# Performance work log

Hardware: AMD Instinct MI355X
Metric: run time of the kernel (lower is better)

## Reference

```python
import jax, jax.numpy as jnp
import numpy as np

BINARY_K = 64  # self.binary_k


def setup_inputs() -> dict:
    key = jax.random.key(0)
    ks = jax.random.split(key, 8)
    R, N, D, H = 8, 128, 512, 256
    obj_feats = jax.random.normal(ks[0], (R, N, D), dtype=jnp.float32)
    geo_feats = jax.random.normal(ks[1], (R, N, N, D), dtype=jnp.float32) * 0.1
    mask = jnp.ones((N, N), dtype=jnp.float32)
    mask = mask.at[jnp.arange(N), jnp.arange(N)].set(0.0)  # zero diagonal, as in forward()
    s1 = 1.0 / np.sqrt(D)
    s2 = 1.0 / np.sqrt(H)
    return {
        "obj_feats": obj_feats,
        "geo_feats": geo_feats,
        "mask": mask,
        "w1a": jax.random.normal(ks[2], (D, H), dtype=jnp.float32) * s1,
        "b1a": jnp.zeros((H,), dtype=jnp.float32),
        "w2a": jax.random.normal(ks[3], (H, 1), dtype=jnp.float32) * s2,
        "b2a": jnp.zeros((1,), dtype=jnp.float32),
        "w1b": jax.random.normal(ks[4], (D, H), dtype=jnp.float32) * s1,
        "b1b": jnp.zeros((H,), dtype=jnp.float32),
        "w2b": jax.random.normal(ks[5], (H, 1), dtype=jnp.float32) * s2,
        "b2b": jnp.zeros((1,), dtype=jnp.float32),
    }


def reference(obj_feats, geo_feats, mask, w1a, b1a, w2a, b2a, w1b, b1b, w2b, b2b):
    # pair_aware_perbatch (dropout = identity in eval mode)
    R, N, D = obj_feats.shape
    k = min(BINARY_K, N * N)

    # pairwise outer-product features + geometric features: [R, N, N, D]
    obj2obj = obj_feats[:, None, :, :] * obj_feats[:, :, None, :] + geo_feats

    # re_clf1 MLP scorer: D -> D/2 -> 1
    h = jax.nn.relu(jnp.einsum('rijd,dh->rijh', obj2obj, w1a) + b1a)
    logits = jnp.einsum('rijh,h->rij', h, w2a[:, 0]) + b2a[0]     # [R, N, N]
    o2o_logits = logits.reshape(R, N * N).sum(axis=0) / R          # [N*N]

    pair_probs = jax.nn.sigmoid(o2o_logits) * mask.ravel()
    _, topk_inds = jax.lax.top_k(pair_probs, k)                    # [k]

    # averaged pair features, gather topk
    a_obj2obj = obj2obj.reshape(R, N * N, D).sum(axis=0) / R       # [N*N, D]
    pair_feats = a_obj2obj[topk_inds]                              # [k, D]

    # pair-of-pair outer product + second MLP scorer
    p2p = pair_feats[None, :, :] * pair_feats[:, None, :]          # [k, k, D]
    h2 = jax.nn.relu(jnp.einsum('ijd,dh->ijh', p2p, w1b) + b1b)
    p2p_logits = jnp.einsum('ijh,h->ij', h2, w2b[:, 0]) + b2b[0]   # [k, k]

    return o2o_logits.reshape(N, N), p2p_logits, topk_inds
```

## Files before the change

### kernel.cpp

```cpp
#include <hip/hip_runtime.h>
#include <math.h>

typedef unsigned int u32;
typedef unsigned long long u64;
typedef unsigned short u16;
typedef short bf16x8 __attribute__((ext_vector_type(8)));
typedef float f32x4 __attribute__((ext_vector_type(4)));

#define RR 8
#define NN 128
#define DD 512
#define HH 256
#define KTOP 64
#define NCAND 256
#define NSEL 128

#define WS_LOGITS_OFF 0
#define WS_CAND_OFF   65536
#define WS_EXACT_OFF  66560
#define WS_CNT_OFF    67584
#define WS_TOPK_OFF   67600
#define WS_PF_OFF     67856
#define WS_WH_OFF     198928
#define WS_WL_OFF     461072

__device__ __forceinline__ u16 bf16rne(float x) {
    union { float f; u32 u; } v; v.f = x;
    u32 r = (v.u + 0x7fffu + ((v.u >> 16) & 1u)) >> 16;
    return (u16)r;
}
__device__ __forceinline__ float bf16tof(u16 h) {
    union { float f; u32 u; } v; v.u = ((u32)h) << 16; return v.f;
}
__device__ __forceinline__ u32 f32sort(float x) {
    union { float f; u32 u; } v; v.f = x;
    return v.u ^ ((v.u & 0x80000000u) ? 0xFFFFFFFFu : 0x80000000u);
}

__global__ __launch_bounds__(256) void k0_splitW(const float* __restrict__ W1,
                                                 u16* __restrict__ wh, u16* __restrict__ wl,
                                                 float* __restrict__ logits)
{
    if (blockIdx.x == 16) {
        float4 z = {0.f, 0.f, 0.f, 0.f};
        for (int t = threadIdx.x; t < 4096; t += 256)
            ((float4*)logits)[t] = z;
        return;
    }
    const int kc = blockIdx.x;
    const int h  = threadIdx.x;
    const int swz = (h >> 1) & 3;
    u16 rh[32], rl[32];
#pragma unroll
    for (int kk = 0; kk < 32; ++kk) {
        float a = W1[(size_t)(kc * 32 + kk) * HH + h];
        u16 hi = bf16rne(a);
        float lo = a - bf16tof(hi);
        rh[kk] = hi; rl[kk] = bf16rne(lo);
    }
    const size_t base = (size_t)kc * 8192 + (size_t)h * 32;
#pragma unroll
    for (int q = 0; q < 4; ++q) {
        uint4 ph, pl;
        ph.x = (u32)rh[q*8+0] | ((u32)rh[q*8+1] << 16);
        ph.y = (u32)rh[q*8+2] | ((u32)rh[q*8+3] << 16);
        ph.z = (u32)rh[q*8+4] | ((u32)rh[q*8+5] << 16);
        ph.w = (u32)rh[q*8+6] | ((u32)rh[q*8+7] << 16);
        pl.x = (u32)rl[q*8+0] | ((u32)rl[q*8+1] << 16);
        pl.y = (u32)rl[q*8+2] | ((u32)rl[q*8+3] << 16);
        pl.z = (u32)rl[q*8+4] | ((u32)rl[q*8+5] << 16);
        pl.w = (u32)rl[q*8+6] | ((u32)rl[q*8+7] << 16);
        const int qs = (q ^ swz) * 8;
        *(uint4*)&wh[base + qs] = ph;
        *(uint4*)&wl[base + qs] = pl;
    }
}

__global__ __launch_bounds__(256, 2) void k1_pair_mfma(
    const float* __restrict__ obj, const float* __restrict__ geo,
    const u16* __restrict__ wh, const u16* __restrict__ wl,
    const float* __restrict__ b1, const float* __restrict__ w2,
    float* __restrict__ logits_acc)
{
    const int jb = blockIdx.x, i = blockIdx.y, r = blockIdx.z;
    const int j0 = jb * 64;
    const int tid = threadIdx.x;
    const int lane = tid & 63, wv = tid >> 6;
    const int l15 = lane & 15, quad = lane >> 4;
    const int fsl = (quad ^ ((l15 >> 1) & 3)) * 8;

    __shared__ float sObjI[DD];
    __shared__ __align__(16) u16 sAh[64 * 32], sAl[64 * 32];
    __shared__ __align__(16) u16 sBh[256 * 32], sBl[256 * 32];

    const float* objI = obj + (size_t)(r * NN + i) * DD;
    for (int t = tid; t < DD; t += 256) sObjI[t] = objI[t];

    f32x4 acc[4][4];
#pragma unroll
    for (int mt = 0; mt < 4; ++mt)
#pragma unroll
        for (int nt = 0; nt < 4; ++nt) acc[mt][nt] = (f32x4){0.f, 0.f, 0.f, 0.f};

    const float* geoB = geo + ((size_t)(r * NN + i) * NN + j0) * DD;
    const float* objJ = obj + (size_t)(r * NN + j0) * DD;

    const int aj = tid >> 2;
    const int ak = (tid & 3) * 8;
    const int asl = ((tid & 3) ^ ((aj >> 1) & 3)) * 8;

    for (int kc = 0; kc < 16; ++kc) {
        const int k0 = kc * 32;
        __syncthreads();
        {
            const char* gh = (const char*)(wh + (size_t)kc * 8192);
            const char* gl = (const char*)(wl + (size_t)kc * 8192);
#pragma unroll
            for (int p = 0; p < 4; ++p) {
                const int off = (wv * 4 + p) * 1024;
                __builtin_amdgcn_global_load_lds(
                    (const __attribute__((address_space(1))) u32*)(gh + off + lane * 16),
                    (__attribute__((address_space(3))) u32*)((char*)sBh + off), 16, 0, 0);
                __builtin_amdgcn_global_load_lds(
                    (const __attribute__((address_space(1))) u32*)(gl + off + lane * 16),
                    (__attribute__((address_space(3))) u32*)((char*)sBl + off), 16, 0, 0);
            }
        }
        {
            float4 g0 = *(const float4*)(geoB + (size_t)aj * DD + k0 + ak);
            float4 g1 = *(const float4*)(geoB + (size_t)aj * DD + k0 + ak + 4);
            float4 o0 = *(const float4*)(objJ + (size_t)aj * DD + k0 + ak);
            float4 o1 = *(const float4*)(objJ + (size_t)aj * DD + k0 + ak + 4);
            float a[8];
            a[0] = fmaf(sObjI[k0+ak+0], o0.x, g0.x);
            a[1] = fmaf(sObjI[k0+ak+1], o0.y, g0.y);
            a[2] = fmaf(sObjI[k0+ak+2], o0.z, g0.z);
            a[3] = fmaf(sObjI[k0+ak+3], o0.w, g0.w);
            a[4] = fmaf(sObjI[k0+ak+4], o1.x, g1.x);
            a[5] = fmaf(sObjI[k0+ak+5], o1.y, g1.y);
            a[6] = fmaf(sObjI[k0+ak+6], o1.z, g1.z);
            a[7] = fmaf(sObjI[k0+ak+7], o1.w, g1.w);
            u16 hs[8], ls[8];
#pragma unroll
            for (int q = 0; q < 8; ++q) {
                hs[q] = bf16rne(a[q]);
                ls[q] = bf16rne(a[q] - bf16tof(hs[q]));
            }
            uint4 ph, pl;
            ph.x = (u32)hs[0] | ((u32)hs[1] << 16); ph.y = (u32)hs[2] | ((u32)hs[3] << 16);
            ph.z = (u32)hs[4] | ((u32)hs[5] << 16); ph.w = (u32)hs[6] | ((u32)hs[7] << 16);
            pl.x = (u32)ls[0] | ((u32)ls[1] << 16); pl.y = (u32)ls[2] | ((u32)ls[3] << 16);
            pl.z = (u32)ls[4] | ((u32)ls[5] << 16); pl.w = (u32)ls[6] | ((u32)ls[7] << 16);
            *(uint4*)&sAh[aj * 32 + asl] = ph;
            *(uint4*)&sAl[aj * 32 + asl] = pl;
        }
        __syncthreads();
        bf16x8 Bh[4], Bl[4], Ah[4], Al[4];
#pragma unroll
        for (int nt = 0; nt < 4; ++nt) {
            const int row = wv * 64 + nt * 16 + l15;
            Bh[nt] = *(const bf16x8*)&sBh[row * 32 + fsl];
            Bl[nt] = *(const bf16x8*)&sBl[row * 32 + fsl];
        }
#pragma unroll
        for (int mt = 0; mt < 4; ++mt) {
            const int row = mt * 16 + l15;
            Ah[mt] = *(const bf16x8*)&sAh[row * 32 + fsl];
            Al[mt] = *(const bf16x8*)&sAl[row * 32 + fsl];
        }
#pragma unroll
        for (int mt = 0; mt < 4; ++mt)
#pragma unroll
            for (int nt = 0; nt < 4; ++nt) {
                acc[mt][nt] = __builtin_amdgcn_mfma_f32_16x16x32_bf16(Ah[mt], Bh[nt], acc[mt][nt], 0, 0, 0);
                acc[mt][nt] = __builtin_amdgcn_mfma_f32_16x16x32_bf16(Ah[mt], Bl[nt], acc[mt][nt], 0, 0, 0);
                acc[mt][nt] = __builtin_amdgcn_mfma_f32_16x16x32_bf16(Al[mt], Bh[nt], acc[mt][nt], 0, 0, 0);
            }
    }
    float pr[4][4];
#pragma unroll
    for (int mt = 0; mt < 4; ++mt)
#pragma unroll
        for (int t = 0; t < 4; ++t) pr[mt][t] = 0.f;
#pragma unroll
    for (int nt = 0; nt < 4; ++nt) {
        const int h = wv * 64 + nt * 16 + l15;
        const float bb = b1[h], w = w2[h];
#pragma unroll
        for (int mt = 0; mt < 4; ++mt)
#pragma unroll
            for (int t = 0; t < 4; ++t)
                pr[mt][t] += fmaxf(acc[mt][nt][t] + bb, 0.f) * w;
    }
#pragma unroll
    for (int mt = 0; mt < 4; ++mt)
#pragma unroll
        for (int t = 0; t < 4; ++t) {
            float v = pr[mt][t];
            v += __shfl_xor(v, 1); v += __shfl_xor(v, 2);
            v += __shfl_xor(v, 4); v += __shfl_xor(v, 8);
            if (l15 == 0)
                atomicAdd(&logits_acc[i * NN + j0 + mt * 16 + quad * 4 + t], v);
        }
}

__global__ __launch_bounds__(1024) void k2_hist(
    const float* __restrict__ logits_acc, const float* __restrict__ mask,
    const float* __restrict__ b2a, float* __restrict__ out,
    int* __restrict__ cand, int* __restrict__ cnt_out)
{
    __shared__ u32 hist[16 * 256];
    __shared__ u32 sum1[256];
    __shared__ int sB1, sRem, sT16;
    __shared__ u32 sCnt;
    const int t = threadIdx.x;
    const int hb = (t >> 6) << 8;
    for (int b = t; b < 16 * 256; b += 1024) hist[b] = 0;
    if (t == 0) sCnt = 0;
    __syncthreads();
    const float bias = b2a[0];
    u32 skey[16];
#pragma unroll
    for (int e = 0; e < 16; ++e) {
        const int idx = e * 1024 + t;
        const float lg = logits_acc[idx] * 0.125f + bias;
        out[idx] = lg;
        u32 s = f32sort(lg);
        if (mask[idx] == 0.f) s = 0;
        skey[e] = s;
        atomicAdd(&hist[hb + (s >> 24)], 1u);
    }
    __syncthreads();
    if (t < 256) {
        u32 s = 0;
#pragma unroll
        for (int c = 0; c < 16; ++c) s += hist[c * 256 + t];
        sum1[t] = s;
    }
    __syncthreads();
    if (t == 0) {
        u32 cum = 0; int b = 255;
        for (; b > 0; --b) { u32 c = sum1[b]; if (cum + c >= (u32)NSEL) break; cum += c; }
        sB1 = b; sRem = NSEL - (int)cum;
    }
    __syncthreads();
    const int B1 = sB1;
    for (int b = t; b < 16 * 256; b += 1024) hist[b] = 0;
    __syncthreads();
#pragma unroll
    for (int e = 0; e < 16; ++e) {
        const u32 s = skey[e];
        if ((int)(s >> 24) == B1) atomicAdd(&hist[hb + ((s >> 16) & 0xFF)], 1u);
    }
    __syncthreads();
    if (t < 256) {
        u32 s = 0;
#pragma unroll
        for (int c = 0; c < 16; ++c) s += hist[c * 256 + t];
        sum1[t] = s;
    }
    __syncthreads();
    if (t == 0) {
        const int rem = sRem; u32 cum = 0; int b = 255;
        for (; b > 0; --b) { cum += sum1[b]; if ((int)cum >= rem) break; }
        sT16 = (B1 << 8) | b;
    }
    __syncthreads();
    const u32 T16 = (u32)sT16;
#pragma unroll
    for (int e = 0; e < 16; ++e) {
        const u32 s = skey[e];
        if (s != 0 && (s >> 16) >= T16) {
            const u32 pos = atomicAdd(&sCnt, 1u);
            if (pos < (u32)NCAND) cand[pos] = e * 1024 + t;
        }
    }
    __syncthreads();
    if (t == 0) *cnt_out = (int)(sCnt < (u32)NCAND ? sCnt : (u32)NCAND);
}

__global__ __launch_bounds__(256) void k5_exact(
    const float* __restrict__ obj, const float* __restrict__ geo,
    const float* __restrict__ W1, const float* __restrict__ b1,
    const float* __restrict__ w2, const float* __restrict__ b2a,
    const int* __restrict__ cand, const int* __restrict__ cnt_ptr,
    float* __restrict__ exact)
{
    const int c = blockIdx.x;
    if (c >= *cnt_ptr) { if (threadIdx.x == 0) exact[c] = -1e30f; return; }
    const int idx = cand[c];
    const int i = idx >> 7, j = idx & 127;
    const int t = threadIdx.x;
    __shared__ float sA[RR][DD];
    __shared__ float sRed[4];
    for (int f = t; f < RR * DD; f += 256) {
        const int r = f >> 9, k = f & 511;
        sA[r][k] = fmaf(obj[(size_t)(r * NN + i) * DD + k],
                        obj[(size_t)(r * NN + j) * DD + k],
                        geo[((size_t)(r * NN + i) * NN + j) * DD + k]);
    }
    __syncthreads();
    float hv[RR];
#pragma unroll
    for (int r = 0; r < RR; ++r) hv[r] = 0.f;
#pragma unroll 8
    for (int k = 0; k < DD; ++k) {
        const float w = W1[(size_t)k * HH + t];
#pragma unroll
        for (int r = 0; r < RR; ++r) hv[r] = fmaf(sA[r][k], w, hv[r]);
    }
    const float bb = b1[t], wv2 = w2[t];
    float p = 0.f;
#pragma unroll
    for (int r = 0; r < RR; ++r) p += fmaxf(hv[r] + bb, 0.f) * wv2;
#pragma unroll
    for (int off = 1; off < 64; off <<= 1) p += __shfl_xor(p, off);
    if ((t & 63) == 0) sRed[t >> 6] = p;
    __syncthreads();
    if (t == 0) exact[c] = (sRed[0] + sRed[1] + sRed[2] + sRed[3]) * 0.125f + b2a[0];
}

__global__ __launch_bounds__(256) void k_sortgather(
    const float* __restrict__ exact, const int* __restrict__ cand,
    const float* __restrict__ obj, const float* __restrict__ geo,
    float* __restrict__ out, float* __restrict__ pf)
{
    __shared__ u64 sKey[NCAND];
    const int t = threadIdx.x;
    {
        const float lg = exact[t];
        u32 ps = 0; u32 idx = 0x7FFFFFFFu;
        if (lg > -1e29f) {
            const float p = 1.f / (1.f + expf(-lg));
            ps = f32sort(p);
            idx = (u32)cand[t];
        }
        sKey[t] = ((u64)ps << 32) | (u64)(0xFFFFFFFFu - idx);
    }
    for (int k = 2; k <= NCAND; k <<= 1)
        for (int j = k >> 1; j > 0; j >>= 1) {
            __syncthreads();
            const int ixj = t ^ j;
            if (ixj > t) {
                const u64 a = sKey[t], b = sKey[ixj];
                if (((t & k) == 0) ? (a < b) : (a > b)) { sKey[t] = b; sKey[ixj] = a; }
            }
        }
    __syncthreads();
    const int tix = blockIdx.x;
    if (tix == 0 && t < KTOP) {
        const u32 oidx = 0xFFFFFFFFu - (u32)(sKey[t] & 0xFFFFFFFFull);
        out[20480 + t] = (float)oidx;
    }
    const int idx = (int)(0xFFFFFFFFu - (u32)(sKey[tix] & 0xFFFFFFFFull));
    const int i = idx >> 7, j = idx & 127;
    for (int dd = t; dd < DD; dd += 256) {
        float s = 0.f;
#pragma unroll
        for (int r = 0; r < RR; ++r) {
            const float oi = obj[(size_t)(r * NN + i) * DD + dd];
            const float oj = obj[(size_t)(r * NN + j) * DD + dd];
            const float g  = geo[((size_t)(r * NN + i) * NN + j) * DD + dd];
            s += oi * oj + g;
        }
        pf[tix * DD + dd] = s * 0.125f;
    }
}

__global__ __launch_bounds__(256) void k4_p2p(
    const float* __restrict__ pf, const float* __restrict__ W1,
    const float* __restrict__ b1, const float* __restrict__ w2,
    const float* __restrict__ b2, float* __restrict__ out)
{
    const int a = blockIdx.x;
    const int tid = threadIdx.x;
    const int lane = tid & 63, wv = tid >> 6;
    const int l15 = lane & 15, quad = lane >> 4;
    const int fsl = (quad ^ ((l15 >> 1) & 3)) * 8;

    __shared__ float sPfA[DD];
    __shared__ __align__(16) u16 sAh[64 * 32], sAl[64 * 32];
    __shared__ __align__(16) u16 sBh[256 * 32], sBl[256 * 32];
    __shared__ float sRed[4][64];

    const float* pfA = pf + (size_t)a * DD;
    for (int t = tid; t < DD; t += 256) sPfA[t] = pfA[t];

    f32x4 acc[4][4];
#pragma unroll
    for (int mt = 0; mt < 4; ++mt)
#pragma unroll
        for (int nt = 0; nt < 4; ++nt) acc[mt][nt] = (f32x4){0.f, 0.f, 0.f, 0.f};

    const int aj = tid >> 2;
    const int ak = (tid & 3) * 8;
    const int asl = ((tid & 3) ^ ((aj >> 1) & 3)) * 8;
    const int swzB = (tid >> 1) & 3;

    for (int kc = 0; kc < 16; ++kc) {
        const int k0 = kc * 32;
        __syncthreads();
        {
            u16 rh[32], rl[32];
#pragma unroll
            for (int kk = 0; kk < 32; ++kk) {
                float w = W1[(size_t)(k0 + kk) * HH + tid];
                u16 hi = bf16rne(w);
                rh[kk] = hi; rl[kk] = bf16rne(w - bf16tof(hi));
            }
#pragma unroll
            for (int q = 0; q < 4; ++q) {
                uint4 ph, pl;
                ph.x = (u32)rh[q*8+0] | ((u32)rh[q*8+1] << 16);
                ph.y = (u32)rh[q*8+2] | ((u32)rh[q*8+3] << 16);
                ph.z = (u32)rh[q*8+4] | ((u32)rh[q*8+5] << 16);
                ph.w = (u32)rh[q*8+6] | ((u32)rh[q*8+7] << 16);
                pl.x = (u32)rl[q*8+0] | ((u32)rl[q*8+1] << 16);
                pl.y = (u32)rl[q*8+2] | ((u32)rl[q*8+3] << 16);
                pl.z = (u32)rl[q*8+4] | ((u32)rl[q*8+5] << 16);
                pl.w = (u32)rl[q*8+6] | ((u32)rl[q*8+7] << 16);
                const int qs = (q ^ swzB) * 8;
                *(uint4*)&sBh[tid * 32 + qs] = ph;
                *(uint4*)&sBl[tid * 32 + qs] = pl;
            }
        }
        {
            float4 p0 = *(const float4*)(pf + (size_t)aj * DD + k0 + ak);
            float4 p1 = *(const float4*)(pf + (size_t)aj * DD + k0 + ak + 4);
            float av[8];
            av[0] = sPfA[k0+ak+0] * p0.x; av[1] = sPfA[k0+ak+1] * p0.y;
            av[2] = sPfA[k0+ak+2] * p0.z; av[3] = sPfA[k0+ak+3] * p0.w;
            av[4] = sPfA[k0+ak+4] * p1.x; av[5] = sPfA[k0+ak+5] * p1.y;
            av[6] = sPfA[k0+ak+6] * p1.z; av[7] = sPfA[k0+ak+7] * p1.w;
            u16 hs[8], ls[8];
#pragma unroll
            for (int q = 0; q < 8; ++q) {
                hs[q] = bf16rne(av[q]);
                ls[q] = bf16rne(av[q] - bf16tof(hs[q]));
            }
            uint4 ph, pl;
            ph.x = (u32)hs[0] | ((u32)hs[1] << 16); ph.y = (u32)hs[2] | ((u32)hs[3] << 16);
            ph.z = (u32)hs[4] | ((u32)hs[5] << 16); ph.w = (u32)hs[6] | ((u32)hs[7] << 16);
            pl.x = (u32)ls[0] | ((u32)ls[1] << 16); pl.y = (u32)ls[2] | ((u32)ls[3] << 16);
            pl.z = (u32)ls[4] | ((u32)ls[5] << 16); pl.w = (u32)ls[6] | ((u32)ls[7] << 16);
            *(uint4*)&sAh[aj * 32 + asl] = ph;
            *(uint4*)&sAl[aj * 32 + asl] = pl;
        }
        __syncthreads();
        bf16x8 Bh[4], Bl[4], Ah[4], Al[4];
#pragma unroll
        for (int nt = 0; nt < 4; ++nt) {
            const int row = wv * 64 + nt * 16 + l15;
            Bh[nt] = *(const bf16x8*)&sBh[row * 32 + fsl];
            Bl[nt] = *(const bf16x8*)&sBl[row * 32 + fsl];
        }
#pragma unroll
        for (int mt = 0; mt < 4; ++mt) {
            const int row = mt * 16 + l15;
            Ah[mt] = *(const bf16x8*)&sAh[row * 32 + fsl];
            Al[mt] = *(const bf16x8*)&sAl[row * 32 + fsl];
        }
#pragma unroll
        for (int mt = 0; mt < 4; ++mt)
#pragma unroll
            for (int nt = 0; nt < 4; ++nt) {
                acc[mt][nt] = __builtin_amdgcn_mfma_f32_16x16x32_bf16(Ah[mt], Bh[nt], acc[mt][nt], 0, 0, 0);
                acc[mt][nt] = __builtin_amdgcn_mfma_f32_16x16x32_bf16(Ah[mt], Bl[nt], acc[mt][nt], 0, 0, 0);
                acc[mt][nt] = __builtin_amdgcn_mfma_f32_16x16x32_bf16(Al[mt], Bh[nt], acc[mt][nt], 0, 0, 0);
                acc[mt][nt] = __builtin_amdgcn_mfma_f32_16x16x32_bf16(Al[mt], Bl[nt], acc[mt][nt], 0, 0, 0);
            }
    }
    float pr[4][4];
#pragma unroll
    for (int mt = 0; mt < 4; ++mt)
#pragma unroll
        for (int t = 0; t < 4; ++t) pr[mt][t] = 0.f;
#pragma unroll
    for (int nt = 0; nt < 4; ++nt) {
        const int h = wv * 64 + nt * 16 + l15;
        const float bb = b1[h], w = w2[h];
#pragma unroll
        for (int mt = 0; mt < 4; ++mt)
#pragma unroll
            for (int t = 0; t < 4; ++t)
                pr[mt][t] += fmaxf(acc[mt][nt][t] + bb, 0.f) * w;
    }
#pragma unroll
    for (int mt = 0; mt < 4; ++mt)
#pragma unroll
        for (int t = 0; t < 4; ++t) {
            float v = pr[mt][t];
            v += __shfl_xor(v, 1); v += __shfl_xor(v, 2);
            v += __shfl_xor(v, 4); v += __shfl_xor(v, 8);
            if (l15 == 0)
                sRed[wv][mt * 16 + quad * 4 + t] = v;
        }
    __syncthreads();
    if (tid < 64)
        out[16384 + a * 64 + tid] =
            sRed[0][tid] + sRed[1][tid] + sRed[2][tid] + sRed[3][tid] + b2[0];
}

extern "C" void kernel_launch(void* const* d_in, const int* in_sizes, int n_in,
                              void* d_out, int out_size, void* d_ws, size_t ws_size,
                              hipStream_t stream) {
    const float* obj  = (const float*)d_in[0];
    const float* geo  = (const float*)d_in[1];
    const float* mask = (const float*)d_in[2];
    const float* w1a  = (const float*)d_in[3];
    const float* b1a  = (const float*)d_in[4];
    const float* w2a  = (const float*)d_in[5];
    const float* b2a  = (const float*)d_in[6];
    const float* w1b  = (const float*)d_in[7];
    const float* b1b  = (const float*)d_in[8];
    const float* w2b  = (const float*)d_in[9];
    const float* b2b  = (const float*)d_in[10];
    float* out = (float*)d_out;

    char* ws = (char*)d_ws;
    float* ws_logits = (float*)(ws + WS_LOGITS_OFF);
    int*   ws_cand   = (int*)  (ws + WS_CAND_OFF);
    float* ws_exact  = (float*)(ws + WS_EXACT_OFF);
    int*   ws_cnt    = (int*)  (ws + WS_CNT_OFF);
    float* ws_pf     = (float*)(ws + WS_PF_OFF);
    u16*   ws_wh     = (u16*)  (ws + WS_WH_OFF);
    u16*   ws_wl     = (u16*)  (ws + WS_WL_OFF);

    k0_splitW<<<17, 256, 0, stream>>>(w1a, ws_wh, ws_wl, ws_logits);
    k1_pair_mfma<<<dim3(2, NN, RR), 256, 0, stream>>>(obj, geo, ws_wh, ws_wl, b1a, w2a, ws_logits);
    k2_hist<<<1, 1024, 0, stream>>>(ws_logits, mask, b2a, out, ws_cand, ws_cnt);
    k5_exact<<<NCAND, 256, 0, stream>>>(obj, geo, w1a, b1a, w2a, b2a, ws_cand, ws_cnt, ws_exact);
    k_sortgather<<<KTOP, 256, 0, stream>>>(ws_exact, ws_cand, obj, geo, out, ws_pf);
    k4_p2p<<<KTOP, 256, 0, stream>>>(ws_pf, w1b, b1b, w2b, b2b, out);
}
```

Measured before the change: 546.0 us.

## Software-pipeline pair-MLP kernel with double-buffered A tiles and prefetched loads

The first pair-scoring MFMA kernel now double-buffers the A (activation) tile in shared memory. It issues the global loads of geo/obj for the next K chunk, plus the async weight staging into LDS, before running the current chunk's MFMAs. Packing the next A tile happens after the MFMAs, so only one barrier is needed per iteration, and MFMA priority is raised with s_setprio. This is meant to hide global-memory latency behind matrix compute. The cost is more LDS and register pressure, and it depends on each wave overwriting only the B rows it already read into registers.

Result: no change. 554.8 us (+1.6%).

```diff
diff --git a/kernel.cpp b/kernel.cpp
--- a/kernel.cpp
+++ b/kernel.cpp
@@ -90,7 +90,7 @@
     const int fsl = (quad ^ ((l15 >> 1) & 3)) * 8;
 
     __shared__ float sObjI[DD];
-    __shared__ __align__(16) u16 sAh[64 * 32], sAl[64 * 32];
+    __shared__ __align__(16) u16 sAh[2][64 * 32], sAl[2][64 * 32];
     __shared__ __align__(16) u16 sBh[256 * 32], sBl[256 * 32];
 
     const float* objI = obj + (size_t)(r * NN + i) * DD;
@@ -109,52 +109,60 @@
     const int ak = (tid & 3) * 8;
     const int asl = ((tid & 3) ^ ((aj >> 1) & 3)) * 8;
 
+#define STAGE_B(KC) do { \
+    const char* gh_ = (const char*)(wh + (size_t)(KC) * 8192); \
+    const char* gl_ = (const char*)(wl + (size_t)(KC) * 8192); \
+    _Pragma("unroll") \
+    for (int p_ = 0; p_ < 4; ++p_) { \
+        const int off_ = (wv * 4 + p_) * 1024; \
+        __builtin_amdgcn_global_load_lds( \
+            (const __attribute__((address_space(1))) u32*)(gh_ + off_ + lane * 16), \
+            (__attribute__((address_space(3))) u32*)((char*)sBh + off_), 16, 0, 0); \
+        __builtin_amdgcn_global_load_lds( \
+            (const __attribute__((address_space(1))) u32*)(gl_ + off_ + lane * 16), \
+            (__attribute__((address_space(3))) u32*)((char*)sBl + off_), 16, 0, 0); \
+    } \
+} while (0)
+
+#define PACK_A(BUF, G0, G1, O0, O1, KBASE) do { \
+    float a_[8]; \
+    a_[0] = fmaf(sObjI[(KBASE)+ak+0], (O0).x, (G0).x); \
+    a_[1] = fmaf(sObjI[(KBASE)+ak+1], (O0).y, (G0).y); \
+    a_[2] = fmaf(sObjI[(KBASE)+ak+2], (O0).z, (G0).z); \
+    a_[3] = fmaf(sObjI[(KBASE)+ak+3], (O0).w, (G0).w); \
+    a_[4] = fmaf(sObjI[(KBASE)+ak+4], (O1).x, (G1).x); \
+    a_[5] = fmaf(sObjI[(KBASE)+ak+5], (O1).y, (G1).y); \
+    a_[6] = fmaf(sObjI[(KBASE)+ak+6], (O1).z, (G1).z); \
+    a_[7] = fmaf(sObjI[(KBASE)+ak+7], (O1).w, (G1).w); \
+    u16 hs_[8], ls_[8]; \
+    _Pragma("unroll") \
+    for (int q_ = 0; q_ < 8; ++q_) { \
+        hs_[q_] = bf16rne(a_[q_]); \
+        ls_[q_] = bf16rne(a_[q_] - bf16tof(hs_[q_])); \
+    } \
+    uint4 ph_, pl_; \
+    ph_.x = (u32)hs_[0] | ((u32)hs_[1] << 16); ph_.y = (u32)hs_[2] | ((u32)hs_[3] << 16); \
+    ph_.z = (u32)hs_[4] | ((u32)hs_[5] << 16); ph_.w = (u32)hs_[6] | ((u32)hs_[7] << 16); \
+    pl_.x = (u32)ls_[0] | ((u32)ls_[1] << 16); pl_.y = (u32)ls_[2] | ((u32)ls_[3] << 16); \
+    pl_.z = (u32)ls_[4] | ((u32)ls_[5] << 16); pl_.w = (u32)ls_[6] | ((u32)ls_[7] << 16); \
+    *(uint4*)&sAh[BUF][aj * 32 + asl] = ph_; \
+    *(uint4*)&sAl[BUF][aj * 32 + asl] = pl_; \
+} while (0)
+
+    STAGE_B(0);
+    __syncthreads();
+    {
+        float4 g0 = *(const float4*)(geoB + (size_t)aj * DD + ak);
+        float4 g1 = *(const float4*)(geoB + (size_t)aj * DD + ak + 4);
+        float4 o0 = *(const float4*)(objJ + (size_t)aj * DD + ak);
+        float4 o1 = *(const float4*)(objJ + (size_t)aj * DD + ak + 4);
+        PACK_A(0, g0, g1, o0, o1, 0);
+    }
+    __syncthreads();
+
+#pragma unroll 1
     for (int kc = 0; kc < 16; ++kc) {
-        const int k0 = kc * 32;
-        __syncthreads();
-        {
-            const char* gh = (const char*)(wh + (size_t)kc * 8192);
-            const char* gl = (const char*)(wl + (size_t)kc * 8192);
-#pragma unroll
-            for (int p = 0; p < 4; ++p) {
-                const int off = (wv * 4 + p) * 1024;
-                __builtin_amdgcn_global_load_lds(
-                    (const __attribute__((address_space(1))) u32*)(gh + off + lane * 16),
-                    (__attribute__((address_space(3))) u32*)((char*)sBh + off), 16, 0, 0);
-                __builtin_amdgcn_global_load_lds(
-                    (const __attribute__((address_space(1))) u32*)(gl + off + lane * 16),
-                    (__attribute__((address_space(3))) u32*)((char*)sBl + off), 16, 0, 0);
-            }
-        }
-        {
-            float4 g0 = *(const float4*)(geoB + (size_t)aj * DD + k0 + ak);
-            float4 g1 = *(const float4*)(geoB + (size_t)aj * DD + k0 + ak + 4);
-            float4 o0 = *(const float4*)(objJ + (size_t)aj * DD + k0 + ak);
-            float4 o1 = *(const float4*)(objJ + (size_t)aj * DD + k0 + ak + 4);
-            float a[8];
-            a[0] = fmaf(sObjI[k0+ak+0], o0.x, g0.x);
-            a[1] = fmaf(sObjI[k0+ak+1], o0.y, g0.y);
-            a[2] = fmaf(sObjI[k0+ak+2], o0.z, g0.z);
-            a[3] = fmaf(sObjI[k0+ak+3], o0.w, g0.w);
-            a[4] = fmaf(sObjI[k0+ak+4], o1.x, g1.x);
-            a[5] = fmaf(sObjI[k0+ak+5], o1.y, g1.y);
-            a[6] = fmaf(sObjI[k0+ak+6], o1.z, g1.z);
-            a[7] = fmaf(sObjI[k0+ak+7], o1.w, g1.w);
-            u16 hs[8], ls[8];
-#pragma unroll
-            for (int q = 0; q < 8; ++q) {
-                hs[q] = bf16rne(a[q]);
-                ls[q] = bf16rne(a[q] - bf16tof(hs[q]));
-            }
-            uint4 ph, pl;
-            ph.x = (u32)hs[0] | ((u32)hs[1] << 16); ph.y = (u32)hs[2] | ((u32)hs[3] << 16);
-            ph.z = (u32)hs[4] | ((u32)hs[5] << 16); ph.w = (u32)hs[6] | ((u32)hs[7] << 16);
-            pl.x = (u32)ls[0] | ((u32)ls[1] << 16); pl.y = (u32)ls[2] | ((u32)ls[3] << 16);
-            pl.z = (u32)ls[4] | ((u32)ls[5] << 16); pl.w = (u32)ls[6] | ((u32)ls[7] << 16);
-            *(uint4*)&sAh[aj * 32 + asl] = ph;
-            *(uint4*)&sAl[aj * 32 + asl] = pl;
-        }
-        __syncthreads();
+        const int cur = kc & 1, nxt = cur ^ 1;
         bf16x8 Bh[4], Bl[4], Ah[4], Al[4];
 #pragma unroll
         for (int nt = 0; nt < 4; ++nt) {
@@ -165,9 +173,22 @@
 #pragma unroll
         for (int mt = 0; mt < 4; ++mt) {
             const int row = mt * 16 + l15;
-            Ah[mt] = *(const bf16x8*)&sAh[row * 32 + fsl];
-            Al[mt] = *(const bf16x8*)&sAl[row * 32 + fsl];
-        }
+            Ah[mt] = *(const bf16x8*)&sAh[cur][row * 32 + fsl];
+            Al[mt] = *(const bf16x8*)&sAl[cur][row * 32 + fsl];
+        }
+        asm volatile("s_waitcnt lgkmcnt(0)" ::: "memory");
+        __builtin_amdgcn_sched_barrier(0);
+        float4 g0, g1, o0, o1;
+        if (kc < 15) {
+            const int kn = (kc + 1) * 32;
+            g0 = *(const float4*)(geoB + (size_t)aj * DD + kn + ak);
+            g1 = *(const float4*)(geoB + (size_t)aj * DD + kn + ak + 4);
+            o0 = *(const float4*)(objJ + (size_t)aj * DD + kn + ak);
+            o1 = *(const float4*)(objJ + (size_t)aj * DD + kn + ak + 4);
+            __builtin_amdgcn_sched_barrier(0);
+            STAGE_B(kc + 1);
+        }
+        __builtin_amdgcn_s_setprio(1);
 #pragma unroll
         for (int mt = 0; mt < 4; ++mt)
 #pragma unroll
@@ -176,7 +197,16 @@
                 acc[mt][nt] = __builtin_amdgcn_mfma_f32_16x16x32_bf16(Ah[mt], Bl[nt], acc[mt][nt], 0, 0, 0);
                 acc[mt][nt] = __builtin_amdgcn_mfma_f32_16x16x32_bf16(Al[mt], Bh[nt], acc[mt][nt], 0, 0, 0);
             }
-    }
+        __builtin_amdgcn_s_setprio(0);
+        if (kc < 15) {
+            const int kn = (kc + 1) * 32;
+            PACK_A(nxt, g0, g1, o0, o1, kn);
+        }
+        __syncthreads();
+    }
+#undef STAGE_B
+#undef PACK_A
+
     float pr[4][4];
 #pragma unroll
     for (int mt = 0; mt < 4; ++mt)
@@ -470,6 +500,7 @@
                 acc[mt][nt] = __builtin_amdgcn_mfma_f32_16x16x32_bf16(Al[mt], Bl[nt], acc[mt][nt], 0, 0, 0);
             }
     }
+    const float b20 = b2[0];
     float pr[4][4];
 #pragma unroll
     for (int mt = 0; mt < 4; ++mt)
@@ -498,7 +529,7 @@
     __syncthreads();
     if (tid < 64)
         out[16384 + a * 64 + tid] =
-            sRed[0][tid] + sRed[1][tid] + sRed[2][tid] + sRed[3][tid] + b2[0];
+            sRed[0][tid] + sRed[1][tid] + sRed[2][tid] + sRed[3][tid] + b20;
 }
 
 extern "C" void kernel_launch(void* const* d_in, const int* in_sizes, int n_in,
```
